# Kernel optimization log

Measured on AMD Instinct MI355X. Metric: run time of the kernel, lower is better.

The kernel has to match this reference:

```python
import jax, jax.numpy as jnp
import numpy as np

NUM_USERS = 100000
NUM_ITEMS = 50000
DIM = 64
N_LAYERS = 3
L_W = 1e-4
E0 = 600000          # raw user-item interactions
B = 8192             # BPR batch size
N_NODES = NUM_USERS + NUM_ITEMS


def setup_inputs() -> dict:
    key = jax.random.key(0)
    k1, k2, k3, k4, k5, k6, k7 = jax.random.split(key, 7)
    return {
        "Gu": jax.random.normal(k1, (NUM_USERS, DIM), jnp.float32) * 0.1,
        "Gi": jax.random.normal(k2, (NUM_ITEMS, DIM), jnp.float32) * 0.1,
        "edge_user": jax.random.randint(k3, (E0,), 0, NUM_USERS),
        "edge_item": jax.random.randint(k4, (E0,), 0, NUM_ITEMS),
        "user": jax.random.randint(k5, (B,), 0, NUM_USERS),
        "pos": jax.random.randint(k6, (B,), 0, NUM_ITEMS),
        "neg": jax.random.randint(k7, (B,), 0, NUM_ITEMS),
    }


def _propagate(Gu, Gi, src, dst):
    # symmetric normalized adjacency (gcn_norm, no self-loops, as in LGConv)
    deg = jax.ops.segment_sum(jnp.ones_like(src, jnp.float32), dst,
                              num_segments=N_NODES)
    dinv = jnp.where(deg > 0, jax.lax.rsqrt(deg), 0.0)
    w = dinv[src] * dinv[dst]                      # [E]
    x = jnp.concatenate([Gu, Gi], axis=0)          # [N, D]
    acc = x
    h = x
    for _ in range(N_LAYERS):
        # SpMM: h' = D^-1/2 A D^-1/2 h  (gather + weighted scatter-add)
        h = jax.ops.segment_sum(w[:, None] * h[src], dst,
                                num_segments=N_NODES)
        acc = acc + h
    emb = acc / (N_LAYERS + 1)                     # mean over all layers
    return emb[:NUM_USERS], emb[NUM_USERS:]


def reference(Gu, Gi, edge_user, edge_item, user, pos, neg):
    # symmetrize bipartite edges; items offset by NUM_USERS
    src = jnp.concatenate([edge_user, edge_item + NUM_USERS])
    dst = jnp.concatenate([edge_item + NUM_USERS, edge_user])
    gu, gi = _propagate(Gu, Gi, src, dst)
    gu_u, gi_p, gi_n = gu[user], gi[pos], gi[neg]  # [B, D]
    xu_pos = jnp.sum(gu_u * gi_p, axis=1)
    xu_neg = jnp.sum(gu_u * gi_n, axis=1)
    mf_loss = -jnp.mean(jax.nn.log_sigmoid(xu_pos - xu_neg))
    reg = L_W * 0.5 * (jnp.sum(gu_u ** 2) + jnp.sum(gi_p ** 2)
                       + jnp.sum(gi_n ** 2)) / B
    return mf_loss + reg
```

## Files before the change

kernel.cpp:

```cpp
#include <hip/hip_runtime.h>

#define NUSERS 100000
#define NITEMS 50000
#define NNODES 150000
#define DIM 64
#define E0 600000
#define E2 (2 * E0)
#define BB 8192
#define LW 1e-4f
#define NN16 150016
#define LOSS_BLOCKS 512
#define SPMM_B 2344
#define SPMMB_B 384

#define NBUCK 1172
#define CHUNK_E 2048
#define CHUNKS 293
#define CPAD 320
#define BCAP 3072

__device__ __forceinline__ float bf_lo(unsigned u) { return __uint_as_float(u << 16); }
__device__ __forceinline__ float bf_hi(unsigned u) { return __uint_as_float(u & 0xffff0000u); }
__device__ __forceinline__ unsigned rne16(float x) {
  unsigned u = __float_as_uint(x);
  return (u + 0x7fffu + ((u >> 16) & 1u)) >> 16;
}
__device__ __forceinline__ unsigned pack2(float lo, float hi) {
  return rne16(lo) | (rne16(hi) << 16);
}

__global__ __launch_bounds__(256) void k_bcount(const int* __restrict__ eu,
                                                const int* __restrict__ ei,
                                                int* __restrict__ cnt) {
  __shared__ int h[NBUCK];
  for (int i = threadIdx.x; i < NBUCK; i += 256) h[i] = 0;
  __syncthreads();
  int c = blockIdx.x;
  int e0 = c * CHUNK_E;
  int e1 = min(e0 + CHUNK_E, E0);
  for (int e = e0 + threadIdx.x; e < e1; e += 256) {
    int u = eu[e];
    int it = NUSERS + ei[e];
    atomicAdd(&h[u >> 7], 1);
    atomicAdd(&h[it >> 7], 1);
  }
  __syncthreads();
  for (int i = threadIdx.x; i < NBUCK; i += 256) cnt[(size_t)i * CPAD + c] = h[i];
}

__global__ __launch_bounds__(256) void k_bscan1(int* __restrict__ cnt,
                                                int* __restrict__ btot) {
  int b = blockIdx.x * 4 + (threadIdx.x >> 6);
  int lane = threadIdx.x & 63;
  int* row = cnt + (size_t)b * CPAD;
  int carry = 0;
  for (int c0 = 0; c0 < CHUNKS; c0 += 64) {
    int c = c0 + lane;
    int v = (c < CHUNKS) ? row[c] : 0;
    int s = v;
    #pragma unroll
    for (int m = 1; m < 64; m <<= 1) {
      int t = __shfl_up(s, m);
      if (lane >= m) s += t;
    }
    if (c < CHUNKS) row[c] = carry + s - v;
    carry += __shfl(s, 63);
  }
  if (lane == 63) btot[b] = carry;
}

__global__ void k_bbase(const int* __restrict__ btot, int* __restrict__ bbase) {
  __shared__ int s[1024];
  int t = threadIdx.x;
  int i0 = 2 * t, i1 = 2 * t + 1;
  int v0 = (i0 < NBUCK) ? btot[i0] : 0;
  int v1 = (i1 < NBUCK) ? btot[i1] : 0;
  s[t] = v0 + v1;
  __syncthreads();
  for (int off = 1; off < 1024; off <<= 1) {
    int x = 0;
    if (t >= off) x = s[t - off];
    __syncthreads();
    if (t >= off) s[t] += x;
    __syncthreads();
  }
  int base = (t > 0) ? s[t - 1] : 0;
  if (i0 < NBUCK) bbase[i0] = base;
  if (i1 < NBUCK) bbase[i1] = base + v0;
}

__global__ __launch_bounds__(256) void k_bscatter(const int* __restrict__ eu,
                                                  const int* __restrict__ ei,
                                                  const int* __restrict__ cnt,
                                                  const int* __restrict__ bbase,
                                                  unsigned* __restrict__ pk) {
  __shared__ int soff[NBUCK];
  int c = blockIdx.x;
  for (int i = threadIdx.x; i < NBUCK; i += 256)
    soff[i] = cnt[(size_t)i * CPAD + c] + bbase[i];
  __syncthreads();
  int e0 = c * CHUNK_E;
  int e1 = min(e0 + CHUNK_E, E0);
  for (int e = e0 + threadIdx.x; e < e1; e += 256) {
    int u = eu[e];
    int it = NUSERS + ei[e];
    int s1 = atomicAdd(&soff[u >> 7], 1);
    pk[s1] = ((unsigned)it << 7) | (unsigned)(u & 127);
    int s2 = atomicAdd(&soff[it >> 7], 1);
    pk[s2] = ((unsigned)u << 7) | (unsigned)(it & 127);
  }
}

__global__ __launch_bounds__(256) void k_bucket_csr(
    const unsigned* __restrict__ pk, const int* __restrict__ btot,
    const int* __restrict__ bbase, int* __restrict__ deg, int* __restrict__ ptr,
    float* __restrict__ dinv, int* __restrict__ col,
    const float4* __restrict__ Gu4, const float4* __restrict__ Gi4,
    uint2* __restrict__ h0) {
  __shared__ unsigned sitm[BCAP];
  __shared__ int ldeg[128], lscan[128], lcnt[128];
  __shared__ float sdv[128];
  int b = blockIdx.x;
  int base = bbase[b];
  int n = btot[b];
  for (int i = threadIdx.x; i < n; i += 256)
    if (i < BCAP) sitm[i] = pk[base + i];
  if (threadIdx.x < 128) { ldeg[threadIdx.x] = 0; lcnt[threadIdx.x] = 0; }
  __syncthreads();
  for (int i = threadIdx.x; i < n; i += 256) {
    unsigned p = (i < BCAP) ? sitm[i] : pk[base + i];
    atomicAdd(&ldeg[p & 127], 1);
  }
  __syncthreads();
  if (threadIdx.x < 128) lscan[threadIdx.x] = ldeg[threadIdx.x];
  __syncthreads();
  for (int off = 1; off < 128; off <<= 1) {
    int t = 0;
    if (threadIdx.x < 128 && (int)threadIdx.x >= off) t = lscan[threadIdx.x - off];
    __syncthreads();
    if (threadIdx.x < 128 && (int)threadIdx.x >= off) lscan[threadIdx.x] += t;
    __syncthreads();
  }
  int node = b * 128 + threadIdx.x;
  if (threadIdx.x < 128) {
    int d = ldeg[threadIdx.x];
    lscan[threadIdx.x] -= d;
    float dv = d > 0 ? rsqrtf((float)d) : 0.0f;
    sdv[threadIdx.x] = dv;
    if (node < NNODES) {
      deg[node] = d;
      ptr[node] = base + lscan[threadIdx.x];
      dinv[node] = dv;
    }
  }
  __syncthreads();
  for (int i = threadIdx.x; i < n; i += 256) {
    unsigned p = (i < BCAP) ? sitm[i] : pk[base + i];
    int dl = p & 127;
    int pos = base + lscan[dl] + atomicAdd(&lcnt[dl], 1);
    col[pos] = (int)(p >> 7);
  }
  for (int w = threadIdx.x; w < 128 * 16; w += 256) {
    int nl = w >> 4, q = w & 15;
    int nd = b * 128 + nl;
    if (nd < NNODES) {
      float dv = sdv[nl];
      float4 v = (nd < NUSERS) ? Gu4[(size_t)nd * 16 + q]
                               : Gi4[(size_t)(nd - NUSERS) * 16 + q];
      h0[(size_t)nd * 16 + q] =
          make_uint2(pack2(dv * v.x, dv * v.y), pack2(dv * v.z, dv * v.w));
    }
  }
}

__global__ __launch_bounds__(512) void k_spmm2(
    const int* __restrict__ ptr, const int* __restrict__ deg,
    const int* __restrict__ col, const float* __restrict__ dinv,
    const uint4* __restrict__ h, uint4* __restrict__ hout) {
  int t = blockIdx.x * 512 + threadIdx.x;
  int g = t >> 3;
  int q = t & 7;
  if (g >= NNODES) return;
  int coff;
  const uint4* hsrc;
  if (g < NUSERS) { coff = NUSERS; hsrc = h + (size_t)NUSERS * 8; }
  else { coff = 0; hsrc = h; }
  int st = ptr[g], dg = deg[g];
  float dn = dinv[g];
  float a0 = 0, a1 = 0, a2 = 0, a3 = 0, a4 = 0, a5 = 0, a6 = 0, a7 = 0;
  int jend = st + dg;
  int j = st;
  for (; j + 2 <= jend; j += 2) {
    int c0 = col[j] - coff;
    int c1 = col[j + 1] - coff;
    uint4 x0 = hsrc[(size_t)c0 * 8 + q];
    uint4 x1 = hsrc[(size_t)c1 * 8 + q];
    a0 += bf_lo(x0.x); a1 += bf_hi(x0.x); a2 += bf_lo(x0.y); a3 += bf_hi(x0.y);
    a4 += bf_lo(x0.z); a5 += bf_hi(x0.z); a6 += bf_lo(x0.w); a7 += bf_hi(x0.w);
    a0 += bf_lo(x1.x); a1 += bf_hi(x1.x); a2 += bf_lo(x1.y); a3 += bf_hi(x1.y);
    a4 += bf_lo(x1.z); a5 += bf_hi(x1.z); a6 += bf_lo(x1.w); a7 += bf_hi(x1.w);
  }
  if (j < jend) {
    int c0 = col[j] - coff;
    uint4 x0 = hsrc[(size_t)c0 * 8 + q];
    a0 += bf_lo(x0.x); a1 += bf_hi(x0.x); a2 += bf_lo(x0.y); a3 += bf_hi(x0.y);
    a4 += bf_lo(x0.z); a5 += bf_hi(x0.z); a6 += bf_lo(x0.w); a7 += bf_hi(x0.w);
  }
  float s = dn * dn;
  hout[(size_t)g * 8 + q] = make_uint4(pack2(a0 * s, a1 * s), pack2(a2 * s, a3 * s),
                                       pack2(a4 * s, a5 * s), pack2(a6 * s, a7 * s));
}

__device__ __forceinline__ int decode_node(int k, const int* __restrict__ usr,
                                           const int* __restrict__ pos,
                                           const int* __restrict__ neg, int* coff) {
  if (k < BB) { *coff = NUSERS; return usr[k]; }
  if (k < 2 * BB) { *coff = 0; return NUSERS + pos[k - BB]; }
  *coff = 0; return NUSERS + neg[k - 2 * BB];
}

__global__ __launch_bounds__(512) void k_spmm_batch(
    const int* __restrict__ usr, const int* __restrict__ pos, const int* __restrict__ neg,
    const int* __restrict__ ptr, const int* __restrict__ deg,
    const int* __restrict__ col, const float* __restrict__ dinv,
    const uint4* __restrict__ h, uint4* __restrict__ hout) {
  int t = blockIdx.x * 512 + threadIdx.x;
  int k = t >> 3;
  int q = t & 7;
  int coff;
  int g = decode_node(k, usr, pos, neg, &coff);
  const uint4* hsrc = h + (size_t)coff * 8;
  int st = ptr[g], dg = deg[g];
  float dn = dinv[g];
  float a0 = 0, a1 = 0, a2 = 0, a3 = 0, a4 = 0, a5 = 0, a6 = 0, a7 = 0;
  int jend = st + dg;
  int j = st;
  for (; j + 2 <= jend; j += 2) {
    int c0 = col[j] - coff;
    int c1 = col[j + 1] - coff;
    uint4 x0 = hsrc[(size_t)c0 * 8 + q];
    uint4 x1 = hsrc[(size_t)c1 * 8 + q];
    a0 += bf_lo(x0.x); a1 += bf_hi(x0.x); a2 += bf_lo(x0.y); a3 += bf_hi(x0.y);
    a4 += bf_lo(x0.z); a5 += bf_hi(x0.z); a6 += bf_lo(x0.w); a7 += bf_hi(x0.w);
    a0 += bf_lo(x1.x); a1 += bf_hi(x1.x); a2 += bf_lo(x1.y); a3 += bf_hi(x1.y);
    a4 += bf_lo(x1.z); a5 += bf_hi(x1.z); a6 += bf_lo(x1.w); a7 += bf_hi(x1.w);
  }
  if (j < jend) {
    int c0 = col[j] - coff;
    uint4 x0 = hsrc[(size_t)c0 * 8 + q];
    a0 += bf_lo(x0.x); a1 += bf_hi(x0.x); a2 += bf_lo(x0.y); a3 += bf_hi(x0.y);
    a4 += bf_lo(x0.z); a5 += bf_hi(x0.z); a6 += bf_lo(x0.w); a7 += bf_hi(x0.w);
  }
  float s = dn * dn;
  hout[(size_t)g * 8 + q] = make_uint4(pack2(a0 * s, a1 * s), pack2(a2 * s, a3 * s),
                                       pack2(a4 * s, a5 * s), pack2(a6 * s, a7 * s));
}

__global__ void k_loss(const int* __restrict__ usr, const int* __restrict__ pos,
                       const int* __restrict__ neg, const int* __restrict__ deg,
                       const float4* __restrict__ Gu4, const float4* __restrict__ Gi4,
                       const uint2* __restrict__ h1, const uint2* __restrict__ h2,
                       const uint2* __restrict__ h3, float* __restrict__ bpart) {
  __shared__ float sL[4], sR[4];
  int wid = threadIdx.x >> 6;
  int lane = threadIdx.x & 63;
  int r = lane >> 4;
  int q = lane & 15;
  int gw = blockIdx.x * 4 + wid;
  int nw = gridDim.x * 4;
  const float s = 0.25f;
  float accL = 0.0f, accR = 0.0f;
  for (int b4 = gw; b4 < BB / 4; b4 += nw) {
    int b = b4 * 4 + r;
    int iu = usr[b], ip = pos[b], ig = neg[b];
    float sdu = sqrtf((float)deg[iu]);
    float sdp = sqrtf((float)deg[NUSERS + ip]);
    float sdn = sqrtf((float)deg[NUSERS + ig]);
    size_t ou = (size_t)iu * 16 + q;
    size_t op = ((size_t)NUSERS + ip) * 16 + q;
    size_t on = ((size_t)NUSERS + ig) * 16 + q;
    float4 u = Gu4[ou];
    float4 p = Gi4[(size_t)ip * 16 + q];
    float4 g = Gi4[(size_t)ig * 16 + q];
    float4 su = {0, 0, 0, 0}, sp = {0, 0, 0, 0}, sg = {0, 0, 0, 0};
    uint2 v;
    v = h1[ou]; su.x += bf_lo(v.x); su.y += bf_hi(v.x); su.z += bf_lo(v.y); su.w += bf_hi(v.y);
    v = h2[ou]; su.x += bf_lo(v.x); su.y += bf_hi(v.x); su.z += bf_lo(v.y); su.w += bf_hi(v.y);
    v = h3[ou]; su.x += bf_lo(v.x); su.y += bf_hi(v.x); su.z += bf_lo(v.y); su.w += bf_hi(v.y);
    v = h1[op]; sp.x += bf_lo(v.x); sp.y += bf_hi(v.x); sp.z += bf_lo(v.y); sp.w += bf_hi(v.y);
    v = h2[op]; sp.x += bf_lo(v.x); sp.y += bf_hi(v.x); sp.z += bf_lo(v.y); sp.w += bf_hi(v.y);
    v = h3[op]; sp.x += bf_lo(v.x); sp.y += bf_hi(v.x); sp.z += bf_lo(v.y); sp.w += bf_hi(v.y);
    v = h1[on]; sg.x += bf_lo(v.x); sg.y += bf_hi(v.x); sg.z += bf_lo(v.y); sg.w += bf_hi(v.y);
    v = h2[on]; sg.x += bf_lo(v.x); sg.y += bf_hi(v.x); sg.z += bf_lo(v.y); sg.w += bf_hi(v.y);
    v = h3[on]; sg.x += bf_lo(v.x); sg.y += bf_hi(v.x); sg.z += bf_lo(v.y); sg.w += bf_hi(v.y);
    u.x = (u.x + sdu * su.x) * s; u.y = (u.y + sdu * su.y) * s;
    u.z = (u.z + sdu * su.z) * s; u.w = (u.w + sdu * su.w) * s;
    p.x = (p.x + sdp * sp.x) * s; p.y = (p.y + sdp * sp.y) * s;
    p.z = (p.z + sdp * sp.z) * s; p.w = (p.w + sdp * sp.w) * s;
    g.x = (g.x + sdn * sg.x) * s; g.y = (g.y + sdn * sg.y) * s;
    g.z = (g.z + sdn * sg.z) * s; g.w = (g.w + sdn * sg.w) * s;
    float dp = u.x * p.x + u.y * p.y + u.z * p.z + u.w * p.w;
    float dn = u.x * g.x + u.y * g.y + u.z * g.z + u.w * g.w;
    float rg = u.x * u.x + u.y * u.y + u.z * u.z + u.w * u.w
             + p.x * p.x + p.y * p.y + p.z * p.z + p.w * p.w
             + g.x * g.x + g.y * g.y + g.z * g.z + g.w * g.w;
    #pragma unroll
    for (int m = 1; m <= 8; m <<= 1) {
      dp += __shfl_xor(dp, m);
      dn += __shfl_xor(dn, m);
      rg += __shfl_xor(rg, m);
    }
    if (q == 0) {
      float diff = dp - dn;
      accL -= fminf(diff, 0.0f) - log1pf(expf(-fabsf(diff)));
      accR += rg;
    }
  }
  accL += __shfl_xor(accL, 16); accR += __shfl_xor(accR, 16);
  accL += __shfl_xor(accL, 32); accR += __shfl_xor(accR, 32);
  if (lane == 0) { sL[wid] = accL; sR[wid] = accR; }
  __syncthreads();
  if (threadIdx.x == 0) {
    bpart[blockIdx.x] = sL[0] + sL[1] + sL[2] + sL[3];
    bpart[LOSS_BLOCKS + blockIdx.x] = sR[0] + sR[1] + sR[2] + sR[3];
  }
}

__global__ void k_final(const float* __restrict__ bpart, float* __restrict__ out) {
  int lane = threadIdx.x;
  float l = 0.0f, r = 0.0f;
  #pragma unroll
  for (int i = 0; i < LOSS_BLOCKS; i += 64) {
    l += bpart[lane + i];
    r += bpart[LOSS_BLOCKS + lane + i];
  }
  for (int off = 32; off > 0; off >>= 1) {
    l += __shfl_down(l, off);
    r += __shfl_down(r, off);
  }
  if (lane == 0) out[0] = l * (1.0f / BB) + LW * 0.5f * r * (1.0f / BB);
}

extern "C" void kernel_launch(void* const* d_in, const int* in_sizes, int n_in,
                              void* d_out, int out_size, void* d_ws, size_t ws_size,
                              hipStream_t stream) {
  const float* Gu = (const float*)d_in[0];
  const float* Gi = (const float*)d_in[1];
  const int* eu  = (const int*)d_in[2];
  const int* ei  = (const int*)d_in[3];
  const int* usr = (const int*)d_in[4];
  const int* pos = (const int*)d_in[5];
  const int* neg = (const int*)d_in[6];
  float* out = (float*)d_out;

  int* deg    = (int*)d_ws;
  int* ptr    = deg + NN16;
  float* dinv = (float*)(ptr + NN16);
  int* col    = (int*)(dinv + NN16);
  uint2* h0   = (uint2*)(col + E2);
  uint2* h1   = h0 + (size_t)NNODES * 16;
  uint2* h2   = h1 + (size_t)NNODES * 16;
  uint2* h3   = h2 + (size_t)NNODES * 16;
  float* bpart = (float*)(h3 + (size_t)NNODES * 16);

  unsigned* pk = (unsigned*)h1;
  int* cnt     = (int*)h2;
  int* btot    = (int*)h3;
  int* bbase   = btot + 1280;

  const float4* Gu4 = (const float4*)Gu;
  const float4* Gi4 = (const float4*)Gi;

  k_bcount<<<CHUNKS, 256, 0, stream>>>(eu, ei, cnt);
  k_bscan1<<<NBUCK / 4, 256, 0, stream>>>(cnt, btot);
  k_bbase<<<1, 1024, 0, stream>>>(btot, bbase);
  k_bscatter<<<CHUNKS, 256, 0, stream>>>(eu, ei, cnt, bbase, pk);
  k_bucket_csr<<<NBUCK, 256, 0, stream>>>(pk, btot, bbase, deg, ptr, dinv, col,
                                          Gu4, Gi4, h0);

  k_spmm2<<<SPMM_B, 512, 0, stream>>>(ptr, deg, col, dinv,
                                      (const uint4*)h0, (uint4*)h1);
  k_spmm2<<<SPMM_B, 512, 0, stream>>>(ptr, deg, col, dinv,
                                      (const uint4*)h1, (uint4*)h2);
  k_spmm_batch<<<SPMMB_B, 512, 0, stream>>>(usr, pos, neg, ptr, deg, col, dinv,
                                            (const uint4*)h2, (uint4*)h3);

  k_loss<<<LOSS_BLOCKS, 256, 0, stream>>>(usr, pos, neg, deg, Gu4, Gi4, h1, h2, h3, bpart);
  k_final<<<1, 64, 0, stream>>>(bpart, out);
}
```

Before: 208.8 us.

## Pre-offset CSR columns, stage column writes in LDS, unroll SpMM by four

The CSR build now stores column indices already shifted into the partition-local index space, so the SpMM kernels no longer subtract an offset per neighbor. It also stages each bucket's column writes in shared memory and writes them out contiguously, which should coalesce the previously scattered global stores. The SpMM gather loops are unrolled by four to keep more loads in flight. The batch SpMM now writes a compact per-batch-slot output that the loss kernel reads directly, avoiding scattered reads of h3; this costs more LDS in the CSR kernel, which may reduce its occupancy.

After: 197.1 us. -5.6%, faster.

```diff
diff --git a/kernel.cpp b/kernel.cpp
--- a/kernel.cpp
+++ b/kernel.cpp
@@ -28,6 +28,11 @@
 __device__ __forceinline__ unsigned pack2(float lo, float hi) {
   return rne16(lo) | (rne16(hi) << 16);
 }
+
+#define ACC8(X) do { \
+    a0 += bf_lo((X).x); a1 += bf_hi((X).x); a2 += bf_lo((X).y); a3 += bf_hi((X).y); \
+    a4 += bf_lo((X).z); a5 += bf_hi((X).z); a6 += bf_lo((X).w); a7 += bf_hi((X).w); \
+  } while (0)
 
 __global__ __launch_bounds__(256) void k_bcount(const int* __restrict__ eu,
                                                 const int* __restrict__ ei,
@@ -118,6 +123,7 @@
     const float4* __restrict__ Gu4, const float4* __restrict__ Gi4,
     uint2* __restrict__ h0) {
   __shared__ unsigned sitm[BCAP];
+  __shared__ int lcol[BCAP];
   __shared__ int ldeg[128], lscan[128], lcnt[128];
   __shared__ float sdv[128];
   int b = blockIdx.x;
@@ -157,9 +163,16 @@
   for (int i = threadIdx.x; i < n; i += 256) {
     unsigned p = (i < BCAP) ? sitm[i] : pk[base + i];
     int dl = p & 127;
-    int pos = base + lscan[dl] + atomicAdd(&lcnt[dl], 1);
-    col[pos] = (int)(p >> 7);
-  }
+    int nb = (int)(p >> 7);
+    int dnode = b * 128 + dl;
+    int val = (dnode < NUSERS) ? nb - NUSERS : nb;
+    int rel = lscan[dl] + atomicAdd(&lcnt[dl], 1);
+    if (rel < BCAP) lcol[rel] = val;
+    else col[base + rel] = val;
+  }
+  __syncthreads();
+  int nf = min(n, BCAP);
+  for (int i = threadIdx.x; i < nf; i += 256) col[base + i] = lcol[i];
   for (int w = threadIdx.x; w < 128 * 16; w += 256) {
     int nl = w >> 4, q = w & 15;
     int nd = b * 128 + nl;
@@ -181,30 +194,31 @@
   int g = t >> 3;
   int q = t & 7;
   if (g >= NNODES) return;
-  int coff;
-  const uint4* hsrc;
-  if (g < NUSERS) { coff = NUSERS; hsrc = h + (size_t)NUSERS * 8; }
-  else { coff = 0; hsrc = h; }
+  const uint4* hq = ((g < NUSERS) ? h + (size_t)NUSERS * 8 : h) + q;
   int st = ptr[g], dg = deg[g];
   float dn = dinv[g];
   float a0 = 0, a1 = 0, a2 = 0, a3 = 0, a4 = 0, a5 = 0, a6 = 0, a7 = 0;
   int jend = st + dg;
   int j = st;
-  for (; j + 2 <= jend; j += 2) {
-    int c0 = col[j] - coff;
-    int c1 = col[j + 1] - coff;
-    uint4 x0 = hsrc[(size_t)c0 * 8 + q];
-    uint4 x1 = hsrc[(size_t)c1 * 8 + q];
-    a0 += bf_lo(x0.x); a1 += bf_hi(x0.x); a2 += bf_lo(x0.y); a3 += bf_hi(x0.y);
-    a4 += bf_lo(x0.z); a5 += bf_hi(x0.z); a6 += bf_lo(x0.w); a7 += bf_hi(x0.w);
-    a0 += bf_lo(x1.x); a1 += bf_hi(x1.x); a2 += bf_lo(x1.y); a3 += bf_hi(x1.y);
-    a4 += bf_lo(x1.z); a5 += bf_hi(x1.z); a6 += bf_lo(x1.w); a7 += bf_hi(x1.w);
+  for (; j + 4 <= jend; j += 4) {
+    int c0 = col[j], c1 = col[j + 1], c2 = col[j + 2], c3 = col[j + 3];
+    uint4 x0 = hq[(size_t)c0 * 8];
+    uint4 x1 = hq[(size_t)c1 * 8];
+    uint4 x2 = hq[(size_t)c2 * 8];
+    uint4 x3 = hq[(size_t)c3 * 8];
+    ACC8(x0); ACC8(x1); ACC8(x2); ACC8(x3);
+  }
+  if (j + 2 <= jend) {
+    int c0 = col[j], c1 = col[j + 1];
+    uint4 x0 = hq[(size_t)c0 * 8];
+    uint4 x1 = hq[(size_t)c1 * 8];
+    ACC8(x0); ACC8(x1);
+    j += 2;
   }
   if (j < jend) {
-    int c0 = col[j] - coff;
-    uint4 x0 = hsrc[(size_t)c0 * 8 + q];
-    a0 += bf_lo(x0.x); a1 += bf_hi(x0.x); a2 += bf_lo(x0.y); a3 += bf_hi(x0.y);
-    a4 += bf_lo(x0.z); a5 += bf_hi(x0.z); a6 += bf_lo(x0.w); a7 += bf_hi(x0.w);
+    int c0 = col[j];
+    uint4 x0 = hq[(size_t)c0 * 8];
+    ACC8(x0);
   }
   float s = dn * dn;
   hout[(size_t)g * 8 + q] = make_uint4(pack2(a0 * s, a1 * s), pack2(a2 * s, a3 * s),
@@ -223,44 +237,48 @@
     const int* __restrict__ usr, const int* __restrict__ pos, const int* __restrict__ neg,
     const int* __restrict__ ptr, const int* __restrict__ deg,
     const int* __restrict__ col, const float* __restrict__ dinv,
-    const uint4* __restrict__ h, uint4* __restrict__ hout) {
+    const uint4* __restrict__ h, uint4* __restrict__ e3) {
   int t = blockIdx.x * 512 + threadIdx.x;
   int k = t >> 3;
   int q = t & 7;
   int coff;
   int g = decode_node(k, usr, pos, neg, &coff);
-  const uint4* hsrc = h + (size_t)coff * 8;
+  const uint4* hq = h + (size_t)coff * 8 + q;
   int st = ptr[g], dg = deg[g];
   float dn = dinv[g];
   float a0 = 0, a1 = 0, a2 = 0, a3 = 0, a4 = 0, a5 = 0, a6 = 0, a7 = 0;
   int jend = st + dg;
   int j = st;
-  for (; j + 2 <= jend; j += 2) {
-    int c0 = col[j] - coff;
-    int c1 = col[j + 1] - coff;
-    uint4 x0 = hsrc[(size_t)c0 * 8 + q];
-    uint4 x1 = hsrc[(size_t)c1 * 8 + q];
-    a0 += bf_lo(x0.x); a1 += bf_hi(x0.x); a2 += bf_lo(x0.y); a3 += bf_hi(x0.y);
-    a4 += bf_lo(x0.z); a5 += bf_hi(x0.z); a6 += bf_lo(x0.w); a7 += bf_hi(x0.w);
-    a0 += bf_lo(x1.x); a1 += bf_hi(x1.x); a2 += bf_lo(x1.y); a3 += bf_hi(x1.y);
-    a4 += bf_lo(x1.z); a5 += bf_hi(x1.z); a6 += bf_lo(x1.w); a7 += bf_hi(x1.w);
+  for (; j + 4 <= jend; j += 4) {
+    int c0 = col[j], c1 = col[j + 1], c2 = col[j + 2], c3 = col[j + 3];
+    uint4 x0 = hq[(size_t)c0 * 8];
+    uint4 x1 = hq[(size_t)c1 * 8];
+    uint4 x2 = hq[(size_t)c2 * 8];
+    uint4 x3 = hq[(size_t)c3 * 8];
+    ACC8(x0); ACC8(x1); ACC8(x2); ACC8(x3);
+  }
+  if (j + 2 <= jend) {
+    int c0 = col[j], c1 = col[j + 1];
+    uint4 x0 = hq[(size_t)c0 * 8];
+    uint4 x1 = hq[(size_t)c1 * 8];
+    ACC8(x0); ACC8(x1);
+    j += 2;
   }
   if (j < jend) {
-    int c0 = col[j] - coff;
-    uint4 x0 = hsrc[(size_t)c0 * 8 + q];
-    a0 += bf_lo(x0.x); a1 += bf_hi(x0.x); a2 += bf_lo(x0.y); a3 += bf_hi(x0.y);
-    a4 += bf_lo(x0.z); a5 += bf_hi(x0.z); a6 += bf_lo(x0.w); a7 += bf_hi(x0.w);
+    int c0 = col[j];
+    uint4 x0 = hq[(size_t)c0 * 8];
+    ACC8(x0);
   }
   float s = dn * dn;
-  hout[(size_t)g * 8 + q] = make_uint4(pack2(a0 * s, a1 * s), pack2(a2 * s, a3 * s),
-                                       pack2(a4 * s, a5 * s), pack2(a6 * s, a7 * s));
+  e3[(size_t)k * 8 + q] = make_uint4(pack2(a0 * s, a1 * s), pack2(a2 * s, a3 * s),
+                                     pack2(a4 * s, a5 * s), pack2(a6 * s, a7 * s));
 }
 
 __global__ void k_loss(const int* __restrict__ usr, const int* __restrict__ pos,
                        const int* __restrict__ neg, const int* __restrict__ deg,
                        const float4* __restrict__ Gu4, const float4* __restrict__ Gi4,
                        const uint2* __restrict__ h1, const uint2* __restrict__ h2,
-                       const uint2* __restrict__ h3, float* __restrict__ bpart) {
+                       const uint2* __restrict__ e3, float* __restrict__ bpart) {
   __shared__ float sL[4], sR[4];
   int wid = threadIdx.x >> 6;
   int lane = threadIdx.x & 63;
@@ -286,13 +304,16 @@
     uint2 v;
     v = h1[ou]; su.x += bf_lo(v.x); su.y += bf_hi(v.x); su.z += bf_lo(v.y); su.w += bf_hi(v.y);
     v = h2[ou]; su.x += bf_lo(v.x); su.y += bf_hi(v.x); su.z += bf_lo(v.y); su.w += bf_hi(v.y);
-    v = h3[ou]; su.x += bf_lo(v.x); su.y += bf_hi(v.x); su.z += bf_lo(v.y); su.w += bf_hi(v.y);
+    v = e3[(size_t)b * 16 + q];
+    su.x += bf_lo(v.x); su.y += bf_hi(v.x); su.z += bf_lo(v.y); su.w += bf_hi(v.y);
     v = h1[op]; sp.x += bf_lo(v.x); sp.y += bf_hi(v.x); sp.z += bf_lo(v.y); sp.w += bf_hi(v.y);
     v = h2[op]; sp.x += bf_lo(v.x); sp.y += bf_hi(v.x); sp.z += bf_lo(v.y); sp.w += bf_hi(v.y);
-    v = h3[op]; sp.x += bf_lo(v.x); sp.y += bf_hi(v.x); sp.z += bf_lo(v.y); sp.w += bf_hi(v.y);
+    v = e3[((size_t)BB + b) * 16 + q];
+    sp.x += bf_lo(v.x); sp.y += bf_hi(v.x); sp.z += bf_lo(v.y); sp.w += bf_hi(v.y);
     v = h1[on]; sg.x += bf_lo(v.x); sg.y += bf_hi(v.x); sg.z += bf_lo(v.y); sg.w += bf_hi(v.y);
     v = h2[on]; sg.x += bf_lo(v.x); sg.y += bf_hi(v.x); sg.z += bf_lo(v.y); sg.w += bf_hi(v.y);
-    v = h3[on]; sg.x += bf_lo(v.x); sg.y += bf_hi(v.x); sg.z += bf_lo(v.y); sg.w += bf_hi(v.y);
+    v = e3[((size_t)2 * BB + b) * 16 + q];
+    sg.x += bf_lo(v.x); sg.y += bf_hi(v.x); sg.z += bf_lo(v.y); sg.w += bf_hi(v.y);
     u.x = (u.x + sdu * su.x) * s; u.y = (u.y + sdu * su.y) * s;
     u.z = (u.z + sdu * su.z) * s; u.w = (u.w + sdu * su.w) * s;
     p.x = (p.x + sdp * sp.x) * s; p.y = (p.y + sdp * sp.y) * s;
@@ -385,6 +406,7 @@
   k_spmm_batch<<<SPMMB_B, 512, 0, stream>>>(usr, pos, neg, ptr, deg, col, dinv,
                                             (const uint4*)h2, (uint4*)h3);
 
-  k_loss<<<LOSS_BLOCKS, 256, 0, stream>>>(usr, pos, neg, deg, Gu4, Gi4, h1, h2, h3, bpart);
+  k_loss<<<LOSS_BLOCKS, 256, 0, stream>>>(usr, pos, neg, deg, Gu4, Gi4, h1, h2,
+                                          (const uint2*)h3, bpart);
   k_final<<<1, 64, 0, stream>>>(bpart, out);
 }
```
